# Kernel optimization log

Hardware: AMD Instinct MI355X
Metric: run time of the kernel (lower is better)

Reference implementation:

```python
import jax, jax.numpy as jnp
import numpy as np


def _layer_norm(x, g, b, eps=1e-5):
    mu = jnp.mean(x, axis=-1, keepdims=True)
    var = jnp.mean((x - mu) ** 2, axis=-1, keepdims=True)
    return (x - mu) * jax.lax.rsqrt(var + eps) * g + b


def setup_inputs() -> dict:
    key = jax.random.key(0)
    ks = jax.random.split(key, 12)
    L, D, HD, F, V, MAXLEN, B, S = 4, 1024, 64, 4096, 32000, 2048, 2, 1024
    s = 0.02
    return {
        "x": jax.random.randint(ks[0], (B, S), 0, V, dtype=jnp.int32),
        "tok_emb": jax.random.normal(ks[1], (V, D), jnp.float32) * s,
        "pos_emb": jax.random.normal(ks[2], (MAXLEN, D), jnp.float32) * s,
        "wq": jax.random.normal(ks[3], (L, HD, HD), jnp.float32) * s,
        "wk": jax.random.normal(ks[4], (L, HD, HD), jnp.float32) * s,
        "wv": jax.random.normal(ks[5], (L, HD, HD), jnp.float32) * s,
        "wo": jax.random.normal(ks[6], (L, D, D), jnp.float32) * s,
        "bo": jnp.zeros((L, D), jnp.float32),
        "ln1_g": jnp.ones((L, D), jnp.float32),
        "ln1_b": jnp.zeros((L, D), jnp.float32),
        "ln2_g": jnp.ones((L, D), jnp.float32),
        "ln2_b": jnp.zeros((L, D), jnp.float32),
        "w1": jax.random.normal(ks[7], (L, F, D), jnp.float32) * s,
        "b1": jnp.zeros((L, F), jnp.float32),
        "w2": jax.random.normal(ks[8], (L, D, F), jnp.float32) * s,
        "b2": jnp.zeros((L, D), jnp.float32),
        "out_w": jax.random.normal(ks[9], (V, D), jnp.float32) * s,
        "out_b": jnp.zeros((V,), jnp.float32),
    }


def reference(x, tok_emb, pos_emb, wq, wk, wv, wo, bo, ln1_g, ln1_b, ln2_g, ln2_b, w1, b1, w2, b2, out_w, out_b):
    B, S = x.shape
    D = tok_emb.shape[1]
    HD = wq.shape[-1]
    H = D // HD
    inv_scale = 1.0 / jnp.sqrt(jnp.asarray(D, jnp.float32))  # note: embed_size, not head_dim

    h = tok_emb[x] + pos_emb[:S][None]  # [B,S,D]; dropout is identity in eval

    def block(h, p):
        pwq, pwk, pwv, pwo, pbo, g1, be1, g2, be2, pw1, pb1, pw2, pb2 = p
        xh = h.reshape(B, S, H, HD)
        # per-head Linear with shared [HD,HD] weight: y = x @ W.T
        q = jnp.einsum('bshd,ed->bshe', xh, pwq)
        k = jnp.einsum('bshd,ed->bshe', xh, pwk)
        v = jnp.einsum('bshd,ed->bshe', xh, pwv)
        energy = jnp.einsum('bqhd,bkhd->bhqk', q, k)  # full [B,H,S,S] scores
        attn = jax.nn.softmax(energy * inv_scale, axis=-1)
        o = jnp.einsum('bhqk,bkhd->bqhd', attn, v).reshape(B, S, D)
        o = o @ pwo.T + pbo
        x1 = _layer_norm(o + h, g1, be1)
        ff = jax.nn.gelu(x1 @ pw1.T + pb1, approximate=False) @ pw2.T + pb2
        return _layer_norm(ff + x1, g2, be2), None

    h, _ = jax.lax.scan(block, h, (wq, wk, wv, wo, bo, ln1_g, ln1_b, ln2_g, ln2_b, w1, b1, w2, b2))
    return h @ out_w.T + out_b  # [B,S,V] logits
```

## Files before the change

kernel.cpp:

```cpp
#include <hip/hip_runtime.h>
#include <math.h>

typedef float f32x4 __attribute__((ext_vector_type(4)));
typedef unsigned short u16x8 __attribute__((ext_vector_type(8)));
typedef unsigned short u16x4 __attribute__((ext_vector_type(4)));
typedef __bf16 bf16x8 __attribute__((ext_vector_type(8)));
typedef unsigned int u32;

#define DEV static __device__ __forceinline__

DEV unsigned short f2bf(float f) {
  unsigned u = __float_as_uint(f);
  u += 0x7FFFu + ((u >> 16) & 1u);
  return (unsigned short)(u >> 16);
}
DEV float bf2f(unsigned short s) { return __uint_as_float(((unsigned)s) << 16); }
DEV bf16x8 asbf(u16x8 v) { return __builtin_bit_cast(bf16x8, v); }

DEV void gload16(const void* g, void* l) {
  __builtin_amdgcn_global_load_lds((const __attribute__((address_space(1))) u32*)g,
                                   (__attribute__((address_space(3))) u32*)l, 16, 0, 0);
}

__global__ void cvt_kernel(const float* __restrict__ in, unsigned short* __restrict__ out, int n8) {
  for (int i = blockIdx.x * 256 + threadIdx.x; i < n8; i += gridDim.x * 256) {
    const float* s = in + (size_t)i * 8;
    f32x4 a = *(const f32x4*)s, b = *(const f32x4*)(s + 4);
    u16x8 o;
    for (int j = 0; j < 4; ++j) { o[j] = f2bf(a[j]); o[j + 4] = f2bf(b[j]); }
    *(u16x8*)(out + (size_t)i * 8) = o;
  }
}

__global__ void embed_kernel(const int* __restrict__ x, const float* __restrict__ tok,
                             const float* __restrict__ pos, float* __restrict__ h,
                             unsigned short* __restrict__ hbf) {
  int t = blockIdx.x, tid = threadIdx.x;
  int v = x[t], s = t & 1023;
  f32x4 a = *(const f32x4*)(tok + (size_t)v * 1024 + tid * 4);
  f32x4 b = *(const f32x4*)(pos + (size_t)s * 1024 + tid * 4);
  f32x4 r = a + b;
  *(f32x4*)(h + (size_t)t * 1024 + tid * 4) = r;
  u16x4 rb;
  for (int i = 0; i < 4; ++i) rb[i] = f2bf(r[i]);
  *(u16x4*)(hbf + (size_t)t * 1024 + tid * 4) = rb;
}

__global__ __launch_bounds__(256) void ln_kernel(const float* __restrict__ preA,
    const float* __restrict__ preB, const float* __restrict__ res,
    const float* __restrict__ g, const float* __restrict__ bta,
    float* __restrict__ outf, unsigned short* __restrict__ outbf) {
  int row = blockIdx.x, tid = threadIdx.x;
  size_t base = (size_t)row * 1024 + tid * 4;
  f32x4 xv = *(const f32x4*)(preA + base);
  xv += *(const f32x4*)(preB + base);
  xv += *(const f32x4*)(res + base);
  float s = xv[0] + xv[1] + xv[2] + xv[3];
  float s2 = xv[0]*xv[0] + xv[1]*xv[1] + xv[2]*xv[2] + xv[3]*xv[3];
  for (int m = 1; m < 64; m <<= 1) { s += __shfl_xor(s, m); s2 += __shfl_xor(s2, m); }
  __shared__ float red[8];
  int w = tid >> 6;
  if ((tid & 63) == 0) { red[w * 2] = s; red[w * 2 + 1] = s2; }
  __syncthreads();
  s = red[0] + red[2] + red[4] + red[6];
  s2 = red[1] + red[3] + red[5] + red[7];
  float mu = s * (1.f / 1024.f);
  float var = s2 * (1.f / 1024.f) - mu * mu;
  float rs = rsqrtf(var + 1e-5f);
  f32x4 gv = *(const f32x4*)(g + tid * 4);
  f32x4 bv = *(const f32x4*)(bta + tid * 4);
  f32x4 o; u16x4 ob;
  for (int i = 0; i < 4; ++i) { o[i] = (xv[i] - mu) * rs * gv[i] + bv[i]; ob[i] = f2bf(o[i]); }
  *(f32x4*)(outf + base) = o;
  *(u16x4*)(outbf + base) = ob;
}

__global__ __launch_bounds__(256) void qkvm_kernel(const unsigned short* __restrict__ hbf,
    const unsigned short* __restrict__ wqb, const unsigned short* __restrict__ wkb,
    const unsigned short* __restrict__ wvb,
    unsigned short* __restrict__ q, unsigned short* __restrict__ k, unsigned short* __restrict__ v) {
  int tid = threadIdx.x, ln = tid & 63, w = tid >> 6;
  int l15 = ln & 15, lg = ln >> 4;
  int st = blockIdx.x, hh = blockIdx.y;
  int t0 = st * 64 + w * 16;
  const unsigned short* xp = hbf + (size_t)(t0 + l15) * 1024 + hh * 64 + lg * 8;
  bf16x8 xa0 = asbf(*(const u16x8*)xp);
  bf16x8 xa1 = asbf(*(const u16x8*)(xp + 32));
  const unsigned short* wp[3] = {wqb, wkb, wvb};
  unsigned short* outp[3] = {q, k, v};
  f32x4 acc[3][4] = {};
#pragma unroll
  for (int m = 0; m < 3; ++m) {
    __builtin_amdgcn_s_setprio(1);
#pragma unroll
    for (int ni = 0; ni < 4; ++ni) {
      const unsigned short* wb = wp[m] + (size_t)(ni * 16 + l15) * 64 + lg * 8;
      bf16x8 w0 = asbf(*(const u16x8*)wb);
      bf16x8 w1 = asbf(*(const u16x8*)(wb + 32));
      acc[m][ni] = __builtin_amdgcn_mfma_f32_16x16x32_bf16(xa0, w0, acc[m][ni], 0, 0, 0);
      acc[m][ni] = __builtin_amdgcn_mfma_f32_16x16x32_bf16(xa1, w1, acc[m][ni], 0, 0, 0);
    }
    __builtin_amdgcn_s_setprio(0);
  }
#pragma unroll
  for (int m = 0; m < 3; ++m)
#pragma unroll
    for (int ni = 0; ni < 4; ++ni)
#pragma unroll
      for (int r = 0; r < 4; ++r)
        outp[m][(size_t)(t0 + 4 * lg + r) * 1024 + hh * 64 + ni * 16 + l15] = f2bf(acc[m][ni][r]);
}

__global__ __launch_bounds__(256) void vtrans_kernel(const unsigned short* __restrict__ v,
                                                     unsigned short* __restrict__ vt) {
  __shared__ unsigned short T[64 * 72];
  int tid = threadIdx.x, st = blockIdx.x, bh = blockIdx.y;
  int b = bh >> 4, hh = bh & 15;
  for (int j = 0; j < 2; ++j) {
    int idx = tid + 256 * j; int s = idx >> 3, e0 = (idx & 7) * 8;
    u16x8 r = *(const u16x8*)(v + ((size_t)(b * 1024 + st * 64 + s) * 16 + hh) * 64 + e0);
    for (int i = 0; i < 8; ++i) T[(e0 + i) * 72 + s] = r[i];
  }
  __syncthreads();
  for (int j = 0; j < 2; ++j) {
    int idx = tid + 256 * j; int e = idx >> 3, s0 = (idx & 7) * 8;
    u16x8 r = *(const u16x8*)(&T[e * 72 + s0]);
    *(u16x8*)(vt + ((size_t)(b * 16 + hh) * 64 + e) * 1024 + st * 64 + s0) = r;
  }
}

__global__ __launch_bounds__(256, 2) void attn_kernel(const unsigned short* __restrict__ qb,
    const unsigned short* __restrict__ kb, const unsigned short* __restrict__ vtb,
    unsigned short* __restrict__ ob) {
  constexpr int PK = 72, PV = 136, PP = 136;
  __shared__ unsigned short Ks[128 * PK], Vs[64 * PV], Ps[4][16 * PP];
  int tid = threadIdx.x, lane = tid & 63, w = tid >> 6;
  int l15 = lane & 15, lg = lane >> 4;
  int qt = blockIdx.x, bh = blockIdx.y, b = bh >> 4, hh = bh & 15;
  int q0 = qt * 64 + w * 16;
  const unsigned short* qrow = qb + ((size_t)(b * 1024 + q0 + l15) * 16 + hh) * 64 + lg * 8;
  bf16x8 qa0 = asbf(*(const u16x8*)qrow);
  bf16x8 qa1 = asbf(*(const u16x8*)(qrow + 32));
  float m_[4] = {-1e30f, -1e30f, -1e30f, -1e30f};
  float ls[4] = {0.f, 0.f, 0.f, 0.f};
  f32x4 oacc[4] = {};
  const float inv = 1.f / 32.f;

  u16x8 KR[4], VR[4];
  auto loadT = [&](int kt) {
#pragma unroll
    for (int j = 0; j < 4; ++j) {
      int idx = tid + 256 * j;
      int r = idx >> 3, c0 = (idx & 7) * 8;
      KR[j] = *(const u16x8*)(kb + ((size_t)(b * 1024 + kt * 128 + r) * 16 + hh) * 64 + c0);
      int rv = idx >> 4, cv = (idx & 15) * 8;
      VR[j] = *(const u16x8*)(vtb + ((size_t)((b * 16 + hh) * 64) + rv) * 1024 + kt * 128 + cv);
    }
  };
  auto writeT = [&]() {
#pragma unroll
    for (int j = 0; j < 4; ++j) {
      int idx = tid + 256 * j;
      int r = idx >> 3, c0 = (idx & 7) * 8;
      *(u16x8*)(&Ks[r * PK + c0]) = KR[j];
      int rv = idx >> 4, cv = (idx & 15) * 8;
      *(u16x8*)(&Vs[rv * PV + cv]) = VR[j];
    }
  };
  loadT(0); writeT();
  __syncthreads();

  for (int kt = 0; kt < 8; ++kt) {
    f32x4 sf[8] = {};
    __builtin_amdgcn_s_setprio(1);
#pragma unroll
    for (int n = 0; n < 8; ++n) {
      bf16x8 k0 = asbf(*(const u16x8*)(&Ks[(n * 16 + l15) * PK + lg * 8]));
      bf16x8 k1 = asbf(*(const u16x8*)(&Ks[(n * 16 + l15) * PK + 32 + lg * 8]));
      sf[n] = __builtin_amdgcn_mfma_f32_16x16x32_bf16(qa0, k0, sf[n], 0, 0, 0);
      sf[n] = __builtin_amdgcn_mfma_f32_16x16x32_bf16(qa1, k1, sf[n], 0, 0, 0);
    }
    __builtin_amdgcn_s_setprio(0);
    if (kt < 7) loadT(kt + 1);
#pragma unroll
    for (int n = 0; n < 8; ++n) sf[n] *= inv;
    float mx[4], sc[4];
#pragma unroll
    for (int r = 0; r < 4; ++r) {
      float t0 = fmaxf(fmaxf(fmaxf(sf[0][r], sf[1][r]), fmaxf(sf[2][r], sf[3][r])),
                       fmaxf(fmaxf(sf[4][r], sf[5][r]), fmaxf(sf[6][r], sf[7][r])));
      for (int msk = 1; msk < 16; msk <<= 1) t0 = fmaxf(t0, __shfl_xor(t0, msk));
      mx[r] = fmaxf(m_[r], t0);
      sc[r] = __expf(m_[r] - mx[r]);
      m_[r] = mx[r];
    }
    float rsum[4] = {0.f, 0.f, 0.f, 0.f};
    unsigned short pb[8][4];
#pragma unroll
    for (int n = 0; n < 8; ++n)
#pragma unroll
      for (int r = 0; r < 4; ++r) {
        float pv = __expf(sf[n][r] - mx[r]);
        rsum[r] += pv;
        pb[n][r] = f2bf(pv);
      }
#pragma unroll
    for (int r = 0; r < 4; ++r) {
      float t0 = rsum[r];
      for (int msk = 1; msk < 16; msk <<= 1) t0 += __shfl_xor(t0, msk);
      ls[r] = ls[r] * sc[r] + t0;
    }
#pragma unroll
    for (int n = 0; n < 4; ++n)
#pragma unroll
      for (int r = 0; r < 4; ++r) oacc[n][r] *= sc[r];
    unsigned short* pw = Ps[w];
#pragma unroll
    for (int n = 0; n < 8; ++n)
#pragma unroll
      for (int r = 0; r < 4; ++r)
        pw[(4 * lg + r) * PP + n * 16 + l15] = pb[n][r];
    asm volatile("s_waitcnt lgkmcnt(0)" ::: "memory");
    __builtin_amdgcn_sched_barrier(0);
    bf16x8 pa[4];
#pragma unroll
    for (int ks = 0; ks < 4; ++ks)
      pa[ks] = asbf(*(const u16x8*)(&pw[l15 * PP + ks * 32 + lg * 8]));
    __builtin_amdgcn_s_setprio(1);
#pragma unroll
    for (int n = 0; n < 4; ++n) {
#pragma unroll
      for (int ks = 0; ks < 4; ++ks) {
        bf16x8 v0 = asbf(*(const u16x8*)(&Vs[(n * 16 + l15) * PV + ks * 32 + lg * 8]));
        oacc[n] = __builtin_amdgcn_mfma_f32_16x16x32_bf16(pa[ks], v0, oacc[n], 0, 0, 0);
      }
    }
    __builtin_amdgcn_s_setprio(0);
    __syncthreads();
    if (kt < 7) { writeT(); __syncthreads(); }
  }
#pragma unroll
  for (int n = 0; n < 4; ++n)
#pragma unroll
    for (int r = 0; r < 4; ++r) {
      float o = oacc[n][r] / ls[r];
      ob[((size_t)(b * 1024 + q0 + 4 * lg + r) * 16 + hh) * 64 + n * 16 + l15] = f2bf(o);
    }
}

template <int BM, int KSPLIT, int EPI>
__global__ __launch_bounds__(256) void gemm_kernel(
    const unsigned short* __restrict__ A, int lda,
    const unsigned short* __restrict__ B, int ldb,
    const float* __restrict__ bias,
    float* __restrict__ CfA, float* __restrict__ CfB, unsigned short* __restrict__ Cb,
    int ldc, int Ksub) {
  constexpr int LOGMT = (BM == 128) ? 4 : 5;
  constexpr int MT = 2048 / BM;
  constexpr int MI = BM / 32;
  __shared__ alignas(16) char smem[33280];
  unsigned short* As = (unsigned short*)smem;
  unsigned short* Bs = As + 2 * BM * 32;
  float* Cs = (float*)smem;

  int wg = blockIdx.x;
  int mt = wg & (MT - 1);
  int rest = wg >> LOGMT;
  int nt, kh;
  if (KSPLIT == 2) { nt = rest & 7; kh = rest >> 3; }
  else { nt = rest; kh = 0; }
  int m0 = mt * BM, n0 = nt * 128;
  const unsigned short* Ae = A + (KSPLIT == 2 ? (size_t)kh * Ksub : 0);
  const unsigned short* Be = B + (KSPLIT == 2 ? (size_t)kh * Ksub : 0);

  int tid = threadIdx.x, ln = tid & 63, wv = tid >> 6;
  int l15 = ln & 15, lg = ln >> 4;
  int wm = (wv >> 1) * (BM / 2), wn = (wv & 1) * 64;

  auto stage = [&](int buf, int k0) {
    for (int j = 0; j < BM / 64; ++j) {
      int row = j * 64 + wv * 16 + (ln >> 2);
      gload16(Ae + (size_t)(m0 + row) * lda + k0 + (ln & 3) * 8,
              &As[buf * (BM * 32) + (j * 64 + wv * 16) * 32]);
    }
    for (int j = 0; j < 2; ++j) {
      int row = j * 64 + wv * 16 + (ln >> 2);
      gload16(Be + (size_t)(n0 + row) * ldb + k0 + (ln & 3) * 8,
              &Bs[buf * 4096 + (j * 64 + wv * 16) * 32]);
    }
  };

  f32x4 acc[MI][4] = {};
  auto compute = [&](int buf) {
    const unsigned short* as = &As[buf * (BM * 32)];
    const unsigned short* bs = &Bs[buf * 4096];
    bf16x8 af[MI], bfn[4];
    for (int mi = 0; mi < MI; ++mi)
      af[mi] = asbf(*(const u16x8*)&as[(wm + mi * 16 + l15) * 32 + lg * 8]);
    for (int ni = 0; ni < 4; ++ni)
      bfn[ni] = asbf(*(const u16x8*)&bs[(wn + ni * 16 + l15) * 32 + lg * 8]);
    for (int mi = 0; mi < MI; ++mi)
      for (int ni = 0; ni < 4; ++ni)
        acc[mi][ni] = __builtin_amdgcn_mfma_f32_16x16x32_bf16(af[mi], bfn[ni], acc[mi][ni], 0, 0, 0);
  };

  stage(0, 0);
  __syncthreads();
  int ntk = Ksub >> 5, cur = 0;
  for (int t = 0; t < ntk - 1; ++t) {
    stage(cur ^ 1, (t + 1) << 5);
    compute(cur);
    __syncthreads();
    cur ^= 1;
  }
  compute(cur);

  float* Cf = (kh == 0) ? CfA : CfB;
  const bool addb = (kh == 0);
  for (int p = 0; p < BM / 64; ++p) {
    __syncthreads();
    if ((wm >> 6) == p) {
      int rb = wm & 63;
      for (int mi = 0; mi < MI; ++mi)
        for (int ni = 0; ni < 4; ++ni) {
          int cn = wn + ni * 16 + l15;
          float bv = addb ? bias[n0 + cn] : 0.f;
          for (int r = 0; r < 4; ++r) {
            float vv = acc[mi][ni][r] + bv;
            if (EPI == 1) vv = 0.5f * vv * (1.f + erff(vv * 0.70710678118f));
            Cs[(rb + mi * 16 + 4 * lg + r) * 130 + cn] = vv;
          }
        }
    }
    __syncthreads();
    int row = tid >> 3;
    for (int ri = 0; ri < 2; ++ri) {
      int lr = ri * 32 + row;
      size_t gbase = (size_t)(m0 + p * 64 + lr) * ldc + n0;
      if (EPI == 0) {
        int c4 = (tid & 7) * 4;
        for (int j = 0; j < 4; ++j)
          *(f32x4*)(Cf + gbase + c4 + j * 32) = *(const f32x4*)&Cs[lr * 130 + c4 + j * 32];
      } else {
        for (int j = 0; j < 2; ++j) {
          int cc = (tid & 7) * 8 + j * 64;
          f32x4 v0 = *(const f32x4*)&Cs[lr * 130 + cc];
          f32x4 v1 = *(const f32x4*)&Cs[lr * 130 + cc + 4];
          u16x8 o;
          for (int i = 0; i < 4; ++i) { o[i] = f2bf(v0[i]); o[i + 4] = f2bf(v1[i]); }
          *(u16x8*)(Cb + gbase + cc) = o;
        }
      }
    }
  }
}

__global__ __launch_bounds__(512, 1) void gemm256_kernel(
    const unsigned short* __restrict__ A, int lda,
    const unsigned short* __restrict__ B, int ldb,
    const float* __restrict__ bias, float* __restrict__ C, int ldc, int K) {
  extern __shared__ unsigned short sm[];
  int b = blockIdx.x;
  int c = (int)gridDim.x >> 3;
  int wg = (b & 7) * c + (b >> 3);
  int mt = wg & 7, nt = wg >> 3;
  int m0 = mt * 256, n0 = nt * 256;

  int tid = threadIdx.x, ln = tid & 63, wv = tid >> 6;
  int l15 = ln & 15, lg = ln >> 4;
  int wm = wv >> 2, wn = wv & 3;
  int l7 = l15 & 7;

  int srow = tid >> 3, sblk = (tid & 7) ^ (srow & 7);
  const unsigned short* Ab = A + (size_t)(m0 + srow) * lda + sblk * 8;
  const unsigned short* BbG[4];
#pragma unroll
  for (int g = 0; g < 4; ++g) {
    int p = g * 64 + srow;
    int j = p & 127;
    int r = ((j >> 5) << 6) + ((p >> 7) << 5) + (j & 31);
    BbG[g] = B + (size_t)(n0 + r) * ldb + sblk * 8;
  }
  auto stA = [&](int e, int g, int k0) {
    gload16(Ab + ((size_t)g * 64) * lda + k0, &sm[e * 16384 + g * 4096 + wv * 512]);
  };
  auto stB = [&](int e, int g, int k0) {
    gload16(BbG[g] + k0, &sm[32768 + e * 16384 + g * 4096 + wv * 512]);
  };

  auto ldsA = [&](int d, int mi, int ks) -> bf16x8 {
    int row = wm * 128 + mi * 16 + l15;
    return asbf(*(const u16x8*)&sm[d * 16384 + row * 64 + (((ks << 2) | lg) ^ l7) * 8]);
  };
  auto ldsB = [&](int d, int ni, int ks) -> bf16x8 {
    int p = ((ni >> 1) << 7) + wn * 32 + ((ni & 1) << 4) + l15;
    return asbf(*(const u16x8*)&sm[32768 + d * 16384 + p * 64 + (((ks << 2) | lg) ^ l7) * 8]);
  };

  f32x4 acc[8][4] = {};
  bf16x8 Af[4][2], Bf01[2][2], Bf23[2][2];

#define PH_OPEN() __builtin_amdgcn_s_barrier(); \
  asm volatile("s_waitcnt lgkmcnt(0)" ::: "memory"); \
  __builtin_amdgcn_sched_barrier(0); __builtin_amdgcn_s_setprio(1)

  stA(0, 0, 0); stA(0, 2, 0); stB(0, 0, 0); stB(0, 1, 0);
  stB(0, 2, 0); stB(0, 3, 0); stA(0, 1, 0); stA(0, 3, 0);
  asm volatile("s_waitcnt vmcnt(0)" ::: "memory");
  __builtin_amdgcn_s_barrier();

  int ntk = K >> 6;
  for (int kk = 0; kk < ntk; ++kk) {
    int d = kk & 1, e = d ^ 1, k1 = (kk + 1) << 6;
    bool pf = (kk + 1 < ntk);
    {
#pragma unroll
      for (int ni = 0; ni < 2; ++ni) { Bf01[ni][0] = ldsB(d, ni, 0); Bf01[ni][1] = ldsB(d, ni, 1); }
#pragma unroll
      for (int mi = 0; mi < 4; ++mi) { Af[mi][0] = ldsA(d, mi, 0); Af[mi][1] = ldsA(d, mi, 1); }
      if (pf) { stA(e, 0, k1); stA(e, 2, k1); stB(e, 0, k1); stB(e, 1, k1); }
      PH_OPEN();
#pragma unroll
      for (int mi = 0; mi < 4; ++mi)
#pragma unroll
        for (int ni = 0; ni < 2; ++ni) {
          acc[mi][ni] = __builtin_amdgcn_mfma_f32_16x16x32_bf16(Af[mi][0], Bf01[ni][0], acc[mi][ni], 0, 0, 0);
          acc[mi][ni] = __builtin_amdgcn_mfma_f32_16x16x32_bf16(Af[mi][1], Bf01[ni][1], acc[mi][ni], 0, 0, 0);
        }
      __builtin_amdgcn_s_setprio(0);
      if (pf) { asm volatile("s_waitcnt vmcnt(6)" ::: "memory"); }
      else    { asm volatile("s_waitcnt vmcnt(2)" ::: "memory"); }
      __builtin_amdgcn_s_barrier();
    }
    {
#pragma unroll
      for (int ni = 0; ni < 2; ++ni) { Bf23[ni][0] = ldsB(d, 2 + ni, 0); Bf23[ni][1] = ldsB(d, 2 + ni, 1); }
      if (pf) { stB(e, 2, k1); stB(e, 3, k1); }
      PH_OPEN();
#pragma unroll
      for (int mi = 0; mi < 4; ++mi)
#pragma unroll
        for (int ni = 0; ni < 2; ++ni) {
          acc[mi][2 + ni] = __builtin_amdgcn_mfma_f32_16x16x32_bf16(Af[mi][0], Bf23[ni][0], acc[mi][2 + ni], 0, 0, 0);
          acc[mi][2 + ni] = __builtin_amdgcn_mfma_f32_16x16x32_bf16(Af[mi][1], Bf23[ni][1], acc[mi][2 + ni], 0, 0, 0);
        }
      __builtin_amdgcn_s_setprio(0);
      if (pf) { asm volatile("s_waitcnt vmcnt(6)" ::: "memory"); }
      else    { asm volatile("s_waitcnt vmcnt(0)" ::: "memory"); }
      __builtin_amdgcn_s_barrier();
    }
    {
#pragma unroll
      for (int mi = 0; mi < 4; ++mi) { Af[mi][0] = ldsA(d, 4 + mi, 0); Af[mi][1] = ldsA(d, 4 + mi, 1); }
      if (pf) { stA(e, 1, k1); stA(e, 3, k1); }
      PH_OPEN();
#pragma unroll
      for (int mi = 0; mi < 4; ++mi)
#pragma unroll
        for (int ni = 0; ni < 2; ++ni) {
          acc[4 + mi][2 + ni] = __builtin_amdgcn_mfma_f32_16x16x32_bf16(Af[mi][0], Bf23[ni][0], acc[4 + mi][2 + ni], 0, 0, 0);
          acc[4 + mi][2 + ni] = __builtin_amdgcn_mfma_f32_16x16x32_bf16(Af[mi][1], Bf23[ni][1], acc[4 + mi][2 + ni], 0, 0, 0);
        }
      __builtin_amdgcn_s_setprio(0);
      __builtin_amdgcn_s_barrier();
    }
    {
      PH_OPEN();
#pragma unroll
      for (int mi = 0; mi < 4; ++mi)
#pragma unroll
        for (int ni = 0; ni < 2; ++ni) {
          acc[4 + mi][ni] = __builtin_amdgcn_mfma_f32_16x16x32_bf16(Af[mi][0], Bf01[ni][0], acc[4 + mi][ni], 0, 0, 0);
          acc[4 + mi][ni] = __builtin_amdgcn_mfma_f32_16x16x32_bf16(Af[mi][1], Bf01[ni][1], acc[4 + mi][ni], 0, 0, 0);
        }
      __builtin_amdgcn_s_setprio(0);
      if (pf) { asm volatile("s_waitcnt vmcnt(4)" ::: "memory"); }
      __builtin_amdgcn_s_barrier();
    }
  }
#undef PH_OPEN

  float* fb = (float*)sm;
  int fbase = wv * 4096;
  float bv[4];
#pragma unroll
  for (int ni = 0; ni < 4; ++ni) bv[ni] = bias[n0 + wn * 64 + ni * 16 + l15];
#pragma unroll
  for (int p = 0; p < 2; ++p) {
    if (p) { asm volatile("s_waitcnt lgkmcnt(0)" ::: "memory"); __builtin_amdgcn_sched_barrier(0); }
#pragma unroll
    for (int mi = 0; mi < 4; ++mi)
#pragma unroll
      for (int ni = 0; ni < 4; ++ni)
#pragma unroll
        for (int r = 0; r < 4; ++r)
          fb[fbase + (mi * 16 + lg * 4 + r) * 64 + ni * 16 + l15] = acc[4 * p + mi][ni][r] + bv[ni];
    asm volatile("s_waitcnt lgkmcnt(0)" ::: "memory");
    __builtin_amdgcn_sched_barrier(0);
#pragma unroll
    for (int i = 0; i < 16; ++i) {
      int row = i * 4 + lg;
      f32x4 v = *(const f32x4*)&fb[fbase + row * 64 + l15 * 4];
      int grow = m0 + wm * 128 + p * 64 + row;
      *(f32x4*)(&C[(size_t)grow * ldc + n0 + wn * 64 + l15 * 4]) = v;
    }
  }
}

extern "C" void kernel_launch(void* const* d_in, const int* in_sizes, int n_in,
                              void* d_out, int out_size, void* d_ws, size_t ws_size,
                              hipStream_t stream) {
  const int* x = (const int*)d_in[0];
  const float* tok = (const float*)d_in[1];
  const float* pos = (const float*)d_in[2];
  const float* wq = (const float*)d_in[3];
  const float* wk = (const float*)d_in[4];
  const float* wv = (const float*)d_in[5];
  const float* wo = (const float*)d_in[6];
  const float* bo = (const float*)d_in[7];
  const float* ln1g = (const float*)d_in[8];
  const float* ln1b = (const float*)d_in[9];
  const float* ln2g = (const float*)d_in[10];
  const float* ln2b = (const float*)d_in[11];
  const float* w1 = (const float*)d_in[12];
  const float* b1 = (const float*)d_in[13];
  const float* w2 = (const float*)d_in[14];
  const float* b2 = (const float*)d_in[15];
  const float* outw = (const float*)d_in[16];
  const float* outb = (const float*)d_in[17];
  float* out = (float*)d_out;

  const size_t MiB = 1 << 20;
  const size_t need = 4 * MiB + 65536000;
  if (ws_size < need) return;
  char* base = (char*)d_ws;
  unsigned short* hbf = (unsigned short*)base;
  char* R = base + 4 * MiB;
  float* hf  = (float*)(R);
  float* x1f = (float*)(R + 8 * MiB);
  unsigned short* x1bf = (unsigned short*)(R + 16 * MiB);
  float* cfA = (float*)(R + 20 * MiB);
  float* cfB = (float*)(R + 28 * MiB);
  unsigned short* qs = (unsigned short*)(R + 36 * MiB);
  const size_t SL = 2048ull * 1024;
  unsigned short* qbf = qs;
  unsigned short* kbf = qs + SL;
  unsigned short* vbf = qs + 2 * SL;
  unsigned short* vtbf = qs + 3 * SL;
  unsigned short* wobf = vtbf;
  unsigned short* w1bf = qbf;
  unsigned short* w2bf = qbf;
  unsigned short* ffbf = vbf;
  unsigned short* wqbf = (unsigned short*)(R + 60 * MiB);
  unsigned short* wkbf = wqbf + 16384;
  unsigned short* wvbf = wkbf + 16384;
  unsigned short* outwbf = (unsigned short*)R;

  embed_kernel<<<2048, 256, 0, stream>>>(x, tok, pos, hf, hbf);
  cvt_kernel<<<8, 256, 0, stream>>>(wq, wqbf, 2048);
  cvt_kernel<<<8, 256, 0, stream>>>(wk, wkbf, 2048);
  cvt_kernel<<<8, 256, 0, stream>>>(wv, wvbf, 2048);
  for (int l = 0; l < 4; ++l) {
    qkvm_kernel<<<dim3(32, 16), 256, 0, stream>>>(hbf, wqbf + l * 4096, wkbf + l * 4096,
                                                  wvbf + l * 4096, qbf, kbf, vbf);
    vtrans_kernel<<<dim3(16, 32), 256, 0, stream>>>(vbf, vtbf);
    attn_kernel<<<dim3(16, 32), 256, 0, stream>>>(qbf, kbf, vtbf, vbf);
    cvt_kernel<<<512, 256, 0, stream>>>(wo + (size_t)l * 1048576, wobf, 131072);
    cvt_kernel<<<2048, 256, 0, stream>>>(w1 + (size_t)l * 4194304, w1bf, 524288);
    gemm_kernel<64, 2, 0><<<512, 256, 0, stream>>>(
        vbf, 1024, wobf, 1024, bo + l * 1024, cfA, cfB, nullptr, 1024, 512);
    ln_kernel<<<2048, 256, 0, stream>>>(cfA, cfB, hf, ln1g + l * 1024, ln1b + l * 1024,
                                        x1f, x1bf);
    gemm_kernel<128, 1, 1><<<512, 256, 0, stream>>>(
        x1bf, 1024, w1bf, 1024, b1 + l * 4096, nullptr, nullptr, ffbf, 4096, 1024);
    cvt_kernel<<<2048, 256, 0, stream>>>(w2 + (size_t)l * 4194304, w2bf, 524288);
    gemm_kernel<64, 2, 0><<<512, 256, 0, stream>>>(
        ffbf, 4096, w2bf, 4096, b2 + l * 1024, cfA, cfB, nullptr, 1024, 2048);
    ln_kernel<<<2048, 256, 0, stream>>>(cfA, cfB, x1f, ln2g + l * 1024, ln2b + l * 1024,
                                        hf, hbf);
  }
  cvt_kernel<<<2048, 256, 0, stream>>>(outw, outwbf, 4096000);
  gemm256_kernel<<<1000, 512, 131072, stream>>>(hbf, 1024, outwbf, 1024, outb, out, 32000, 1024);
}
```

Baseline: 891.5 us.

## Fuse V transpose into QKV kernel, merge weight conversions, replace output GEMM

The QKV projection kernel now transposes V through shared memory and writes the transposed layout directly, which removes the separate vtrans kernel and one round trip of V through global memory. The wo and w1 fp32-to-bf16 conversions are merged into a single launch. The specialized 256x256 output-projection GEMM is deleted and replaced by the generic 128-row gemm_kernel with a new block-index swizzle option, launched with 4000 workgroups. Dropping the hand-pipelined 256-tile kernel for the largest GEMM risks lower MFMA efficiency and less data reuse on the logits projection.

Result: slower. 922.4 us (+3.5%).

```diff
diff --git a/kernel.cpp b/kernel.cpp
--- a/kernel.cpp
+++ b/kernel.cpp
@@ -29,6 +29,19 @@
     u16x8 o;
     for (int j = 0; j < 4; ++j) { o[j] = f2bf(a[j]); o[j + 4] = f2bf(b[j]); }
     *(u16x8*)(out + (size_t)i * 8) = o;
+  }
+}
+
+__global__ void cvt2_kernel(const float* __restrict__ s0, unsigned short* __restrict__ d0, int na,
+                            const float* __restrict__ s1, unsigned short* __restrict__ d1, int nb) {
+  int total = na + nb;
+  for (int i = blockIdx.x * 256 + threadIdx.x; i < total; i += gridDim.x * 256) {
+    const float* s; unsigned short* d; int k;
+    if (i < na) { s = s0; d = d0; k = i; } else { s = s1; d = d1; k = i - na; }
+    f32x4 a = *(const f32x4*)(s + (size_t)k * 8), b = *(const f32x4*)(s + (size_t)k * 8 + 4);
+    u16x8 o;
+    for (int j = 0; j < 4; ++j) { o[j] = f2bf(a[j]); o[j + 4] = f2bf(b[j]); }
+    *(u16x8*)(d + (size_t)k * 8) = o;
   }
 }
 
@@ -75,10 +88,12 @@
   *(u16x4*)(outbf + base) = ob;
 }
 
-__global__ __launch_bounds__(256) void qkvm_kernel(const unsigned short* __restrict__ hbf,
+__global__ __launch_bounds__(256) void qkvt_kernel(const unsigned short* __restrict__ hbf,
     const unsigned short* __restrict__ wqb, const unsigned short* __restrict__ wkb,
     const unsigned short* __restrict__ wvb,
-    unsigned short* __restrict__ q, unsigned short* __restrict__ k, unsigned short* __restrict__ v) {
+    unsigned short* __restrict__ q, unsigned short* __restrict__ k,
+    unsigned short* __restrict__ vt) {
+  __shared__ unsigned short T[64 * 72];
   int tid = threadIdx.x, ln = tid & 63, w = tid >> 6;
   int l15 = ln & 15, lg = ln >> 4;
   int st = blockIdx.x, hh = blockIdx.y;
@@ -87,7 +102,6 @@
   bf16x8 xa0 = asbf(*(const u16x8*)xp);
   bf16x8 xa1 = asbf(*(const u16x8*)(xp + 32));
   const unsigned short* wp[3] = {wqb, wkb, wvb};
-  unsigned short* outp[3] = {q, k, v};
   f32x4 acc[3][4] = {};
 #pragma unroll
   for (int m = 0; m < 3; ++m) {
@@ -102,30 +116,26 @@
     }
     __builtin_amdgcn_s_setprio(0);
   }
-#pragma unroll
-  for (int m = 0; m < 3; ++m)
+  unsigned short* outp[2] = {q, k};
+#pragma unroll
+  for (int m = 0; m < 2; ++m)
 #pragma unroll
     for (int ni = 0; ni < 4; ++ni)
 #pragma unroll
       for (int r = 0; r < 4; ++r)
         outp[m][(size_t)(t0 + 4 * lg + r) * 1024 + hh * 64 + ni * 16 + l15] = f2bf(acc[m][ni][r]);
-}
-
-__global__ __launch_bounds__(256) void vtrans_kernel(const unsigned short* __restrict__ v,
-                                                     unsigned short* __restrict__ vt) {
-  __shared__ unsigned short T[64 * 72];
-  int tid = threadIdx.x, st = blockIdx.x, bh = blockIdx.y;
-  int b = bh >> 4, hh = bh & 15;
+#pragma unroll
+  for (int ni = 0; ni < 4; ++ni)
+#pragma unroll
+    for (int r = 0; r < 4; ++r)
+      T[(ni * 16 + l15) * 72 + (w * 16 + 4 * lg + r)] = f2bf(acc[2][ni][r]);
+  __syncthreads();
+  int b = st >> 4, sb = (st & 15) * 64;
+#pragma unroll
   for (int j = 0; j < 2; ++j) {
-    int idx = tid + 256 * j; int s = idx >> 3, e0 = (idx & 7) * 8;
-    u16x8 r = *(const u16x8*)(v + ((size_t)(b * 1024 + st * 64 + s) * 16 + hh) * 64 + e0);
-    for (int i = 0; i < 8; ++i) T[(e0 + i) * 72 + s] = r[i];
-  }
-  __syncthreads();
-  for (int j = 0; j < 2; ++j) {
-    int idx = tid + 256 * j; int e = idx >> 3, s0 = (idx & 7) * 8;
-    u16x8 r = *(const u16x8*)(&T[e * 72 + s0]);
-    *(u16x8*)(vt + ((size_t)(b * 16 + hh) * 64 + e) * 1024 + st * 64 + s0) = r;
+    int idx = tid + 256 * j; int e = idx >> 3, s8 = (idx & 7) * 8;
+    *(u16x8*)(vt + ((size_t)((b * 16 + hh) * 64 + e)) * 1024 + sb + s8) =
+        *(const u16x8*)&T[e * 72 + s8];
   }
 }
 
@@ -248,7 +258,7 @@
     }
 }
 
-template <int BM, int KSPLIT, int EPI>
+template <int BM, int KSPLIT, int EPI, int SWZ>
 __global__ __launch_bounds__(256) void gemm_kernel(
     const unsigned short* __restrict__ A, int lda,
     const unsigned short* __restrict__ B, int ldb,
@@ -264,6 +274,7 @@
   float* Cs = (float*)smem;
 
   int wg = blockIdx.x;
+  if (SWZ) { int ch = (int)gridDim.x >> 3; wg = (wg & 7) * ch + (wg >> 3); }
   int mt = wg & (MT - 1);
   int rest = wg >> LOGMT;
   int nt, kh;
@@ -351,158 +362,6 @@
           *(u16x8*)(Cb + gbase + cc) = o;
         }
       }
-    }
-  }
-}
-
-__global__ __launch_bounds__(512, 1) void gemm256_kernel(
-    const unsigned short* __restrict__ A, int lda,
-    const unsigned short* __restrict__ B, int ldb,
-    const float* __restrict__ bias, float* __restrict__ C, int ldc, int K) {
-  extern __shared__ unsigned short sm[];
-  int b = blockIdx.x;
-  int c = (int)gridDim.x >> 3;
-  int wg = (b & 7) * c + (b >> 3);
-  int mt = wg & 7, nt = wg >> 3;
-  int m0 = mt * 256, n0 = nt * 256;
-
-  int tid = threadIdx.x, ln = tid & 63, wv = tid >> 6;
-  int l15 = ln & 15, lg = ln >> 4;
-  int wm = wv >> 2, wn = wv & 3;
-  int l7 = l15 & 7;
-
-  int srow = tid >> 3, sblk = (tid & 7) ^ (srow & 7);
-  const unsigned short* Ab = A + (size_t)(m0 + srow) * lda + sblk * 8;
-  const unsigned short* BbG[4];
-#pragma unroll
-  for (int g = 0; g < 4; ++g) {
-    int p = g * 64 + srow;
-    int j = p & 127;
-    int r = ((j >> 5) << 6) + ((p >> 7) << 5) + (j & 31);
-    BbG[g] = B + (size_t)(n0 + r) * ldb + sblk * 8;
-  }
-  auto stA = [&](int e, int g, int k0) {
-    gload16(Ab + ((size_t)g * 64) * lda + k0, &sm[e * 16384 + g * 4096 + wv * 512]);
-  };
-  auto stB = [&](int e, int g, int k0) {
-    gload16(BbG[g] + k0, &sm[32768 + e * 16384 + g * 4096 + wv * 512]);
-  };
-
-  auto ldsA = [&](int d, int mi, int ks) -> bf16x8 {
-    int row = wm * 128 + mi * 16 + l15;
-    return asbf(*(const u16x8*)&sm[d * 16384 + row * 64 + (((ks << 2) | lg) ^ l7) * 8]);
-  };
-  auto ldsB = [&](int d, int ni, int ks) -> bf16x8 {
-    int p = ((ni >> 1) << 7) + wn * 32 + ((ni & 1) << 4) + l15;
-    return asbf(*(const u16x8*)&sm[32768 + d * 16384 + p * 64 + (((ks << 2) | lg) ^ l7) * 8]);
-  };
-
-  f32x4 acc[8][4] = {};
-  bf16x8 Af[4][2], Bf01[2][2], Bf23[2][2];
-
-#define PH_OPEN() __builtin_amdgcn_s_barrier(); \
-  asm volatile("s_waitcnt lgkmcnt(0)" ::: "memory"); \
-  __builtin_amdgcn_sched_barrier(0); __builtin_amdgcn_s_setprio(1)
-
-  stA(0, 0, 0); stA(0, 2, 0); stB(0, 0, 0); stB(0, 1, 0);
-  stB(0, 2, 0); stB(0, 3, 0); stA(0, 1, 0); stA(0, 3, 0);
-  asm volatile("s_waitcnt vmcnt(0)" ::: "memory");
-  __builtin_amdgcn_s_barrier();
-
-  int ntk = K >> 6;
-  for (int kk = 0; kk < ntk; ++kk) {
-    int d = kk & 1, e = d ^ 1, k1 = (kk + 1) << 6;
-    bool pf = (kk + 1 < ntk);
-    {
-#pragma unroll
-      for (int ni = 0; ni < 2; ++ni) { Bf01[ni][0] = ldsB(d, ni, 0); Bf01[ni][1] = ldsB(d, ni, 1); }
-#pragma unroll
-      for (int mi = 0; mi < 4; ++mi) { Af[mi][0] = ldsA(d, mi, 0); Af[mi][1] = ldsA(d, mi, 1); }
-      if (pf) { stA(e, 0, k1); stA(e, 2, k1); stB(e, 0, k1); stB(e, 1, k1); }
-      PH_OPEN();
-#pragma unroll
-      for (int mi = 0; mi < 4; ++mi)
-#pragma unroll
-        for (int ni = 0; ni < 2; ++ni) {
-          acc[mi][ni] = __builtin_amdgcn_mfma_f32_16x16x32_bf16(Af[mi][0], Bf01[ni][0], acc[mi][ni], 0, 0, 0);
-          acc[mi][ni] = __builtin_amdgcn_mfma_f32_16x16x32_bf16(Af[mi][1], Bf01[ni][1], acc[mi][ni], 0, 0, 0);
-        }
-      __builtin_amdgcn_s_setprio(0);
-      if (pf) { asm volatile("s_waitcnt vmcnt(6)" ::: "memory"); }
-      else    { asm volatile("s_waitcnt vmcnt(2)" ::: "memory"); }
-      __builtin_amdgcn_s_barrier();
-    }
-    {
-#pragma unroll
-      for (int ni = 0; ni < 2; ++ni) { Bf23[ni][0] = ldsB(d, 2 + ni, 0); Bf23[ni][1] = ldsB(d, 2 + ni, 1); }
-      if (pf) { stB(e, 2, k1); stB(e, 3, k1); }
-      PH_OPEN();
-#pragma unroll
-      for (int mi = 0; mi < 4; ++mi)
-#pragma unroll
-        for (int ni = 0; ni < 2; ++ni) {
-          acc[mi][2 + ni] = __builtin_amdgcn_mfma_f32_16x16x32_bf16(Af[mi][0], Bf23[ni][0], acc[mi][2 + ni], 0, 0, 0);
-          acc[mi][2 + ni] = __builtin_amdgcn_mfma_f32_16x16x32_bf16(Af[mi][1], Bf23[ni][1], acc[mi][2 + ni], 0, 0, 0);
-        }
-      __builtin_amdgcn_s_setprio(0);
-      if (pf) { asm volatile("s_waitcnt vmcnt(6)" ::: "memory"); }
-      else    { asm volatile("s_waitcnt vmcnt(0)" ::: "memory"); }
-      __builtin_amdgcn_s_barrier();
-    }
-    {
-#pragma unroll
-      for (int mi = 0; mi < 4; ++mi) { Af[mi][0] = ldsA(d, 4 + mi, 0); Af[mi][1] = ldsA(d, 4 + mi, 1); }
-      if (pf) { stA(e, 1, k1); stA(e, 3, k1); }
-      PH_OPEN();
-#pragma unroll
-      for (int mi = 0; mi < 4; ++mi)
-#pragma unroll
-        for (int ni = 0; ni < 2; ++ni) {
-          acc[4 + mi][2 + ni] = __builtin_amdgcn_mfma_f32_16x16x32_bf16(Af[mi][0], Bf23[ni][0], acc[4 + mi][2 + ni], 0, 0, 0);
-          acc[4 + mi][2 + ni] = __builtin_amdgcn_mfma_f32_16x16x32_bf16(Af[mi][1], Bf23[ni][1], acc[4 + mi][2 + ni], 0, 0, 0);
-        }
-      __builtin_amdgcn_s_setprio(0);
-      __builtin_amdgcn_s_barrier();
-    }
-    {
-      PH_OPEN();
-#pragma unroll
-      for (int mi = 0; mi < 4; ++mi)
-#pragma unroll
-        for (int ni = 0; ni < 2; ++ni) {
-          acc[4 + mi][ni] = __builtin_amdgcn_mfma_f32_16x16x32_bf16(Af[mi][0], Bf01[ni][0], acc[4 + mi][ni], 0, 0, 0);
-          acc[4 + mi][ni] = __builtin_amdgcn_mfma_f32_16x16x32_bf16(Af[mi][1], Bf01[ni][1], acc[4 + mi][ni], 0, 0, 0);
-        }
-      __builtin_amdgcn_s_setprio(0);
-      if (pf) { asm volatile("s_waitcnt vmcnt(4)" ::: "memory"); }
-      __builtin_amdgcn_s_barrier();
-    }
-  }
-#undef PH_OPEN
-
-  float* fb = (float*)sm;
-  int fbase = wv * 4096;
-  float bv[4];
-#pragma unroll
-  for (int ni = 0; ni < 4; ++ni) bv[ni] = bias[n0 + wn * 64 + ni * 16 + l15];
-#pragma unroll
-  for (int p = 0; p < 2; ++p) {
-    if (p) { asm volatile("s_waitcnt lgkmcnt(0)" ::: "memory"); __builtin_amdgcn_sched_barrier(0); }
-#pragma unroll
-    for (int mi = 0; mi < 4; ++mi)
-#pragma unroll
-      for (int ni = 0; ni < 4; ++ni)
-#pragma unroll
-        for (int r = 0; r < 4; ++r)
-          fb[fbase + (mi * 16 + lg * 4 + r) * 64 + ni * 16 + l15] = acc[4 * p + mi][ni][r] + bv[ni];
-    asm volatile("s_waitcnt lgkmcnt(0)" ::: "memory");
-    __builtin_amdgcn_sched_barrier(0);
-#pragma unroll
-    for (int i = 0; i < 16; ++i) {
-      int row = i * 4 + lg;
-      f32x4 v = *(const f32x4*)&fb[fbase + row * 64 + l15 * 4];
-      int grow = m0 + wm * 128 + p * 64 + row;
-      *(f32x4*)(&C[(size_t)grow * ldc + n0 + wn * 64 + l15 * 4]) = v;
     }
   }
 }
@@ -561,24 +420,24 @@
   cvt_kernel<<<8, 256, 0, stream>>>(wk, wkbf, 2048);
   cvt_kernel<<<8, 256, 0, stream>>>(wv, wvbf, 2048);
   for (int l = 0; l < 4; ++l) {
-    qkvm_kernel<<<dim3(32, 16), 256, 0, stream>>>(hbf, wqbf + l * 4096, wkbf + l * 4096,
-                                                  wvbf + l * 4096, qbf, kbf, vbf);
-    vtrans_kernel<<<dim3(16, 32), 256, 0, stream>>>(vbf, vtbf);
+    qkvt_kernel<<<dim3(32, 16), 256, 0, stream>>>(hbf, wqbf + l * 4096, wkbf + l * 4096,
+                                                  wvbf + l * 4096, qbf, kbf, vtbf);
     attn_kernel<<<dim3(16, 32), 256, 0, stream>>>(qbf, kbf, vtbf, vbf);
-    cvt_kernel<<<512, 256, 0, stream>>>(wo + (size_t)l * 1048576, wobf, 131072);
-    cvt_kernel<<<2048, 256, 0, stream>>>(w1 + (size_t)l * 4194304, w1bf, 524288);
-    gemm_kernel<64, 2, 0><<<512, 256, 0, stream>>>(
+    cvt2_kernel<<<2048, 256, 0, stream>>>(wo + (size_t)l * 1048576, wobf, 131072,
+                                          w1 + (size_t)l * 4194304, w1bf, 524288);
+    gemm_kernel<64, 2, 0, 0><<<512, 256, 0, stream>>>(
         vbf, 1024, wobf, 1024, bo + l * 1024, cfA, cfB, nullptr, 1024, 512);
     ln_kernel<<<2048, 256, 0, stream>>>(cfA, cfB, hf, ln1g + l * 1024, ln1b + l * 1024,
                                         x1f, x1bf);
-    gemm_kernel<128, 1, 1><<<512, 256, 0, stream>>>(
+    gemm_kernel<128, 1, 1, 0><<<512, 256, 0, stream>>>(
         x1bf, 1024, w1bf, 1024, b1 + l * 4096, nullptr, nullptr, ffbf, 4096, 1024);
     cvt_kernel<<<2048, 256, 0, stream>>>(w2 + (size_t)l * 4194304, w2bf, 524288);
-    gemm_kernel<64, 2, 0><<<512, 256, 0, stream>>>(
+    gemm_kernel<64, 2, 0, 0><<<512, 256, 0, stream>>>(
         ffbf, 4096, w2bf, 4096, b2 + l * 1024, cfA, cfB, nullptr, 1024, 2048);
     ln_kernel<<<2048, 256, 0, stream>>>(cfA, cfB, x1f, ln2g + l * 1024, ln2b + l * 1024,
                                         hf, hbf);
   }
   cvt_kernel<<<2048, 256, 0, stream>>>(outw, outwbf, 4096000);
-  gemm256_kernel<<<1000, 512, 131072, stream>>>(hbf, 1024, outwbf, 1024, outb, out, 32000, 1024);
-}
+  gemm_kernel<128, 1, 0, 1><<<4000, 256, 0, stream>>>(
+      hbf, 1024, outwbf, 1024, outb, out, nullptr, nullptr, 32000, 1024);
+}
```
